# Kernel tuning notes

Hardware: AMD Instinct MI355X
Metric: run time of the kernel (lower is better)

## Reference

```python
import jax, jax.numpy as jnp
import numpy as np

N_C = 50000
N_N = 50000
E = 500000
D = 128


def _graph_conv(x_src, src, dst, n_src, n_dst, W, b):
    # DGL GraphConv, norm='both': symmetric degree normalization, then linear.
    ones = jnp.ones(src.shape, x_src.dtype)
    deg_out = jax.ops.segment_sum(ones, src, num_segments=n_src)
    deg_in = jax.ops.segment_sum(ones, dst, num_segments=n_dst)
    norm_src = jnp.maximum(deg_out, 1.0) ** -0.5  # [n_src]
    norm_dst = jnp.maximum(deg_in, 1.0) ** -0.5   # [n_dst]
    m = (x_src * norm_src[:, None])[src]          # [E, D] gather
    agg = jax.ops.segment_sum(m, dst, num_segments=n_dst)  # [n_dst, D]
    return (agg * norm_dst[:, None]) @ W + b


def _sage_conv(x_src, x_dst, src, dst, n_dst, W_self, W_neigh, b):
    # DGL SAGEConv, aggregator='mean': fc_self(h_dst) + fc_neigh(mean_neigh) + bias.
    ones = jnp.ones(src.shape, x_src.dtype)
    deg_in = jnp.maximum(jax.ops.segment_sum(ones, dst, num_segments=n_dst), 1.0)
    h_neigh = jax.ops.segment_sum(x_src[src], dst, num_segments=n_dst) / deg_in[:, None]
    return x_dst @ W_self + h_neigh @ W_neigh + b


def setup_inputs() -> dict:
    key = jax.random.key(0)
    ks = jax.random.split(key, 20)
    s = 1.0 / np.sqrt(D)
    inp = {
        'feat_C': jax.random.normal(ks[0], (N_C, D), jnp.float32),
        'feat_N': jax.random.normal(ks[1], (N_N, D), jnp.float32),
        'W1_cc': jax.random.normal(ks[2], (D, D), jnp.float32) * s,
        'b1_cc': jnp.zeros((D,), jnp.float32),
        'W1_cn': jax.random.normal(ks[3], (D, D), jnp.float32) * s,
        'b1_cn': jnp.zeros((D,), jnp.float32),
        'W1_self': jax.random.normal(ks[4], (D, D), jnp.float32) * s,
        'W1_neigh': jax.random.normal(ks[5], (D, D), jnp.float32) * s,
        'b1_nn': jnp.zeros((D,), jnp.float32),
        'W2_cc': jax.random.normal(ks[6], (D, D), jnp.float32) * s,
        'b2_cc': jnp.zeros((D,), jnp.float32),
        'W2_cn': jax.random.normal(ks[7], (D, D), jnp.float32) * s,
        'b2_cn': jnp.zeros((D,), jnp.float32),
        'W2_self': jax.random.normal(ks[8], (D, D), jnp.float32) * s,
        'W2_neigh': jax.random.normal(ks[9], (D, D), jnp.float32) * s,
        'b2_nn': jnp.zeros((D,), jnp.float32),
        'cc_src': jax.random.randint(ks[10], (E,), 0, N_C),
        'cc_dst': jax.random.randint(ks[11], (E,), 0, N_C),
        'cn_src': jax.random.randint(ks[12], (E,), 0, N_C),
        'cn_dst': jax.random.randint(ks[13], (E,), 0, N_N),
        'nn_src': jax.random.randint(ks[14], (E,), 0, N_N),
        'nn_dst': jax.random.randint(ks[15], (E,), 0, N_N),
    }
    return inp


def reference(feat_C, feat_N, W1_cc, b1_cc, W1_cn, b1_cn, W1_self, W1_neigh, b1_nn,
              W2_cc, b2_cc, W2_cn, b2_cn, W2_self, W2_neigh, b2_nn,
              cc_src, cc_dst, cn_src, cn_dst, nn_src, nn_dst):
    # layer 1 (HeteroGraphConv, aggregate='sum') + relu
    hC = _graph_conv(feat_C, cc_src, cc_dst, N_C, N_C, W1_cc, b1_cc)
    hN = (_graph_conv(feat_C, cn_src, cn_dst, N_C, N_N, W1_cn, b1_cn)
          + _sage_conv(feat_N, feat_N, nn_src, nn_dst, N_N, W1_self, W1_neigh, b1_nn))
    hC = jax.nn.relu(hC)
    hN = jax.nn.relu(hN)
    # layer 2
    oC = _graph_conv(hC, cc_src, cc_dst, N_C, N_C, W2_cc, b2_cc)
    oN = (_graph_conv(hC, cn_src, cn_dst, N_C, N_N, W2_cn, b2_cn)
          + _sage_conv(hN, hN, nn_src, nn_dst, N_N, W2_self, W2_neigh, b2_nn))
    return oC, oN
```

## Files before the change

kernel.cpp:

```cpp
#include <hip/hip_runtime.h>

#define NCN 50000
#define NE  500000
#define DF  128

#define BSHIFT 9
#define NBUCK 98
#define BK 128
#define CAP 7168
#define CHUNK 4096

typedef __attribute__((ext_vector_type(8))) short mfrag;
typedef __attribute__((ext_vector_type(4))) float facc4;

__device__ inline ushort f2bf(float x) {
    unsigned u = __float_as_uint(x);
    unsigned r = (u + 0x7FFFu + ((u >> 16) & 1u)) >> 16;
    return (ushort)r;
}
__device__ inline float bf2f(ushort h) { return __uint_as_float(((unsigned)h) << 16); }

__device__ inline void store_split(ushort* __restrict__ T, int row, int lane,
                                   float vx, float vy) {
    ushort hx = f2bf(vx); ushort lx = f2bf(vx - bf2f(hx));
    ushort hy = f2bf(vy); ushort ly = f2bf(vy - bf2f(hy));
    uint hp = (uint)hx | ((uint)hy << 16);
    uint lp = (uint)lx | ((uint)ly << 16);
    *(uint*)(T + (size_t)row * DF + lane * 2) = hp;
    *(uint*)(T + (size_t)NCN * DF + (size_t)row * DF + lane * 2) = lp;
}

__global__ __launch_bounds__(256) void binA_k(
    const int* __restrict__ cc_src, const int* __restrict__ cc_dst,
    const int* __restrict__ cn_src, const int* __restrict__ cn_dst,
    const int* __restrict__ nn_src, const int* __restrict__ nn_dst,
    uint2* __restrict__ R, int* __restrict__ bc)
{
    const int s = blockIdx.y;
    const int* key; const int* pay;
    switch (s) {
      case 0: key = cc_dst; pay = cc_src; break;
      case 1: key = cn_dst; pay = cn_src; break;
      case 2: key = nn_dst; pay = nn_src; break;
      case 3: key = cc_src; pay = nullptr; break;
      default: key = cn_src; pay = nullptr; break;
    }
    __shared__ uint2 rec[CHUNK];
    __shared__ int lhist[BK], lofs[BK], lcur[BK], gbase[BK];
    __shared__ int ls[256];
    const int tid = threadIdx.x;
    const int base = blockIdx.x * CHUNK;

    int k[16], p[16];
    #pragma unroll
    for (int j = 0; j < 16; ++j) {
        int e = base + j * 256 + tid;
        bool valid = (e < NE);
        k[j] = valid ? key[e] : -1;
        p[j] = (valid && pay) ? pay[e] : 0;
    }
    if (tid < BK) lhist[tid] = 0;
    __syncthreads();
    #pragma unroll
    for (int j = 0; j < 16; ++j)
        if (k[j] >= 0) atomicAdd(&lhist[k[j] >> BSHIFT], 1);
    __syncthreads();
    int v = (tid < BK) ? lhist[tid] : 0;
    ls[tid] = v;
    __syncthreads();
    #pragma unroll
    for (int off = 1; off < 128; off <<= 1) {
        int t = (tid >= off) ? ls[tid - off] : 0;
        __syncthreads();
        ls[tid] += t;
        __syncthreads();
    }
    if (tid < BK) { int e = ls[tid] - v; lofs[tid] = e; lcur[tid] = e; }
    __syncthreads();
    #pragma unroll
    for (int j = 0; j < 16; ++j) {
        if (k[j] >= 0) {
            int b = k[j] >> BSHIFT;
            int pos = atomicAdd(&lcur[b], 1);
            rec[pos] = make_uint2((unsigned)k[j], (unsigned)p[j]);
        }
    }
    __syncthreads();
    if (tid < BK) {
        int c = lcur[tid] - lofs[tid];
        gbase[tid] = (c > 0) ? atomicAdd(&bc[s * BK + tid], c) : 0;
    }
    __syncthreads();
    int total = ls[127];
    for (int i = tid; i < total; i += 256) {
        uint2 r = rec[i];
        int b = (int)(r.x >> BSHIFT);
        int gi = gbase[b] + (i - lofs[b]);
        R[((size_t)s * NBUCK + b) * CAP + gi] = r;
    }
}

__global__ __launch_bounds__(256) void binB_k(
    const uint2* __restrict__ R, const int* __restrict__ bc,
    int* __restrict__ rp3, int* __restrict__ col3, float* __restrict__ snorm2)
{
    const int b = blockIdx.x;
    const int s = blockIdx.y;
    const int tid = threadIdx.x;
    __shared__ int cnt[512];
    __shared__ int lofs[512];
    __shared__ int ls[256];
    __shared__ int sbase;

    const int nrec = bc[s * BK + b];
    const uint2* rec = R + ((size_t)s * NBUCK + b) * CAP;

    for (int i = tid; i < 512; i += 256) cnt[i] = 0;
    __syncthreads();
    for (int i = tid; i < nrec; i += 256)
        atomicAdd(&cnt[rec[i].x & 511], 1);
    __syncthreads();

    if (s >= 3) {
        float* sn = snorm2 + (size_t)(s - 3) * NCN;
        for (int j = tid; j < 512; j += 256) {
            int d = b * 512 + j;
            if (d < NCN) { int c = cnt[j]; if (c < 1) c = 1; sn[d] = rsqrtf((float)c); }
        }
        return;
    }

    {
        int v = (tid < b) ? bc[s * BK + tid] : 0;
        ls[tid] = v;
        __syncthreads();
        for (int off = 128; off > 0; off >>= 1) {
            if (tid < off) ls[tid] += ls[tid + off];
            __syncthreads();
        }
        if (tid == 0) sbase = ls[0];
        __syncthreads();
    }
    const int colBase = sbase;

    int v0 = cnt[2 * tid], v1 = cnt[2 * tid + 1];
    int pairSum = v0 + v1;
    ls[tid] = pairSum;
    __syncthreads();
    #pragma unroll
    for (int off = 1; off < 256; off <<= 1) {
        int t = (tid >= off) ? ls[tid - off] : 0;
        __syncthreads();
        ls[tid] += t;
        __syncthreads();
    }
    int excl = ls[tid] - pairSum;
    lofs[2 * tid] = excl;
    lofs[2 * tid + 1] = excl + v0;
    __syncthreads();
    const int total = ls[255];

    int* rp = rp3 + (size_t)s * (NCN + 1);
    for (int j = tid; j < 512; j += 256) {
        int d = b * 512 + j;
        if (d < NCN) rp[d] = colBase + lofs[j];
    }
    if (b == NBUCK - 1 && tid == 0) rp[NCN] = colBase + total;
    __syncthreads();

    int* col = col3 + (size_t)s * NE + colBase;
    for (int i = tid; i < nrec; i += 256) {
        uint2 r = rec[i];
        int pos = atomicAdd(&lofs[r.x & 511], 1);
        col[pos] = (int)r.y;
    }
}

__global__ __launch_bounds__(256) void wconv_k(
    const float* __restrict__ Wm0, const float* __restrict__ Wm1,
    const float* __restrict__ Wm2, const float* __restrict__ Wm3,
    const float* __restrict__ Wm4, const float* __restrict__ Wm5,
    const float* __restrict__ Wm6, const float* __restrict__ Wm7,
    ushort* __restrict__ out)
{
    const float* Ws[8] = {Wm0, Wm1, Wm2, Wm3, Wm4, Wm5, Wm6, Wm7};
    const float* W = Ws[blockIdx.x];
    ushort* o = out + (size_t)blockIdx.x * 32768;
    for (int i = threadIdx.x; i < 16384; i += 256) {
        int c = i >> 13;
        int r = i & 8191;
        int n = r >> 6;
        int jj = r & 63;
        int kk = c * 64 + (jj ^ ((n & 7) << 3));
        float wv = W[kk * 128 + n];
        ushort h = f2bf(wv);
        float lv = wv - bf2f(h);
        o[c * 16384 + r] = h;
        o[c * 16384 + 8192 + r] = f2bf(lv);
    }
}

__global__ __launch_bounds__(256) void agg2_k(
    const float* __restrict__ X,
    const int* __restrict__ rpA, const int* __restrict__ colA,
    const float* __restrict__ scA, ushort* __restrict__ outA,
    const int* __restrict__ rpB, const int* __restrict__ colB,
    const float* __restrict__ scB, ushort* __restrict__ outB)
{
    const int* rp; const int* col; const float* sc; ushort* out;
    if (blockIdx.y == 0) { rp = rpA; col = colA; sc = scA; out = outA; }
    else                 { rp = rpB; col = colB; sc = scB; out = outB; }
    int gid = blockIdx.x * 256 + threadIdx.x;
    int row = gid >> 6;
    int lane = threadIdx.x & 63;
    if (row >= NCN) return;
    int e0 = rp[row], e1 = rp[row + 1];
    float ax = 0.f, ay = 0.f;
    int e = e0;
    for (; e + 4 <= e1; e += 4) {
        int s0 = col[e], s1 = col[e + 1], s2 = col[e + 2], s3 = col[e + 3];
        float c0 = sc[s0], c1 = sc[s1], c2 = sc[s2], c3 = sc[s3];
        const float2 u0 = *(const float2*)(X + (size_t)s0 * DF + lane * 2);
        const float2 u1 = *(const float2*)(X + (size_t)s1 * DF + lane * 2);
        const float2 u2 = *(const float2*)(X + (size_t)s2 * DF + lane * 2);
        const float2 u3 = *(const float2*)(X + (size_t)s3 * DF + lane * 2);
        ax = fmaf(u0.x, c0, ax); ay = fmaf(u0.y, c0, ay);
        ax = fmaf(u1.x, c1, ax); ay = fmaf(u1.y, c1, ay);
        ax = fmaf(u2.x, c2, ax); ay = fmaf(u2.y, c2, ay);
        ax = fmaf(u3.x, c3, ax); ay = fmaf(u3.y, c3, ay);
    }
    for (; e < e1; ++e) {
        int s0 = col[e];
        float c0 = sc[s0];
        const float2 u0 = *(const float2*)(X + (size_t)s0 * DF + lane * 2);
        ax = fmaf(u0.x, c0, ax); ay = fmaf(u0.y, c0, ay);
    }
    int deg = e1 - e0; if (deg < 1) deg = 1;
    float dsc = rsqrtf((float)deg);
    store_split(out, row, lane, ax * dsc, ay * dsc);
}

__global__ __launch_bounds__(256) void agg1_k(
    const float* __restrict__ X, const int* __restrict__ rp,
    const int* __restrict__ col, ushort* __restrict__ out)
{
    int gid = blockIdx.x * 256 + threadIdx.x;
    int row = gid >> 6;
    int lane = threadIdx.x & 63;
    if (row >= NCN) return;
    int e0 = rp[row], e1 = rp[row + 1];
    float ax = 0.f, ay = 0.f;
    int e = e0;
    for (; e + 4 <= e1; e += 4) {
        int s0 = col[e], s1 = col[e + 1], s2 = col[e + 2], s3 = col[e + 3];
        const float2 u0 = *(const float2*)(X + (size_t)s0 * DF + lane * 2);
        const float2 u1 = *(const float2*)(X + (size_t)s1 * DF + lane * 2);
        const float2 u2 = *(const float2*)(X + (size_t)s2 * DF + lane * 2);
        const float2 u3 = *(const float2*)(X + (size_t)s3 * DF + lane * 2);
        ax += u0.x + u1.x + u2.x + u3.x;
        ay += u0.y + u1.y + u2.y + u3.y;
    }
    for (; e < e1; ++e) {
        int s0 = col[e];
        const float2 u0 = *(const float2*)(X + (size_t)s0 * DF + lane * 2);
        ax += u0.x; ay += u0.y;
    }
    int deg = e1 - e0; if (deg < 1) deg = 1;
    float dsc = 1.0f / (float)deg;
    store_split(out, row, lane, ax * dsc, ay * dsc);
}

template<int NSRC, bool RELU, int F32S>
__global__ __launch_bounds__(256, 3) void mgemm_k(
    const void* __restrict__ A0, const void* __restrict__ A1, const void* __restrict__ A2,
    const ushort* __restrict__ Wi0, const ushort* __restrict__ Wi1, const ushort* __restrict__ Wi2,
    const float* __restrict__ b0, const float* __restrict__ b1,
    float* __restrict__ Y, int M)
{
    constexpr int NCH = 2 * NSRC;
    __shared__ ushort Wsm[16384];
    const int tid = threadIdx.x;
    const int l = tid & 63;
    const int wv = tid >> 6;
    const int r0 = blockIdx.x * 128;

    const void*   Aarr[3] = {A0, A1, A2};
    const ushort* Warr[3] = {Wi0, Wi1, Wi2};

    int arow[2];
    #pragma unroll
    for (int rt = 0; rt < 2; ++rt) {
        int r = r0 + wv * 32 + rt * 16 + (l & 15);
        arow[rt] = (r < M) ? r : (M - 1);
    }
    const int kgrp = (l >> 4) * 8;

    facc4 acc[2][8];
    #pragma unroll
    for (int rt = 0; rt < 2; ++rt)
        #pragma unroll
        for (int ct = 0; ct < 8; ++ct)
            acc[rt][ct] = (facc4){0.f, 0.f, 0.f, 0.f};

    uint4 Wr[8];
    auto loadWr = [&](int c) {
        int s = c >> 1, half = c & 1;
        const uint4* wp = (const uint4*)(Warr[s] + half * 16384);
        #pragma unroll
        for (int i = 0; i < 8; ++i) Wr[i] = wp[i * 256 + tid];
    };

    mfrag ah[2][2], al[2][2];
    auto loadA = [&](int c) {
        int s = c >> 1;
        int k0 = (c & 1) * 64;
        if (s == F32S) {
            const float* F = (const float*)Aarr[s];
            #pragma unroll
            for (int ks = 0; ks < 2; ++ks)
                #pragma unroll
                for (int rt = 0; rt < 2; ++rt) {
                    const float* p = F + (size_t)arow[rt] * DF + k0 + ks * 32 + kgrp;
                    float4 v0 = *(const float4*)p;
                    float4 v1 = *(const float4*)(p + 4);
                    union { mfrag m; ushort u[8]; } H, L;
                    float vv0[4] = {v0.x, v0.y, v0.z, v0.w};
                    float vv1[4] = {v1.x, v1.y, v1.z, v1.w};
                    #pragma unroll
                    for (int j = 0; j < 4; ++j) {
                        ushort h = f2bf(vv0[j]);
                        H.u[j] = h; L.u[j] = f2bf(vv0[j] - bf2f(h));
                    }
                    #pragma unroll
                    for (int j = 0; j < 4; ++j) {
                        ushort h = f2bf(vv1[j]);
                        H.u[4 + j] = h; L.u[4 + j] = f2bf(vv1[j] - bf2f(h));
                    }
                    ah[ks][rt] = H.m; al[ks][rt] = L.m;
                }
        } else {
            const ushort* T = (const ushort*)Aarr[s];
            #pragma unroll
            for (int ks = 0; ks < 2; ++ks)
                #pragma unroll
                for (int rt = 0; rt < 2; ++rt) {
                    size_t o = (size_t)arow[rt] * DF + k0 + ks * 32 + kgrp;
                    ah[ks][rt] = *(const mfrag*)(T + o);
                    al[ks][rt] = *(const mfrag*)(T + (size_t)NCN * DF + o);
                }
        }
    };

    loadWr(0);
    #pragma unroll
    for (int c = 0; c < NCH; ++c) {
        __syncthreads();
        {
            uint4* wd = (uint4*)Wsm;
            #pragma unroll
            for (int i = 0; i < 8; ++i) wd[i * 256 + tid] = Wr[i];
        }
        loadA(c);
        if (c + 1 < NCH) loadWr(c + 1);
        __syncthreads();
        #pragma unroll
        for (int ks = 0; ks < 2; ++ks) {
            const int kbyte = ks * 64 + (l >> 4) * 16;
            #pragma unroll
            for (int ct = 0; ct < 8; ++ct) {
                int colc = ct * 16 + (l & 15);
                int widx = colc * 64 + ((kbyte ^ ((colc & 7) << 4)) >> 1);
                mfrag w_hi = *(const mfrag*)(Wsm + widx);
                mfrag w_lo = *(const mfrag*)(Wsm + 8192 + widx);
                #pragma unroll
                for (int rt = 0; rt < 2; ++rt) {
                    acc[rt][ct] = __builtin_amdgcn_mfma_f32_16x16x32_bf16(ah[ks][rt], w_hi, acc[rt][ct], 0, 0, 0);
                    acc[rt][ct] = __builtin_amdgcn_mfma_f32_16x16x32_bf16(ah[ks][rt], w_lo, acc[rt][ct], 0, 0, 0);
                    acc[rt][ct] = __builtin_amdgcn_mfma_f32_16x16x32_bf16(al[ks][rt], w_hi, acc[rt][ct], 0, 0, 0);
                }
            }
        }
    }

    float bias[8];
    #pragma unroll
    for (int ct = 0; ct < 8; ++ct) {
        int colc = ct * 16 + (l & 15);
        float bv = b0 ? b0[colc] : 0.f;
        if (b1) bv += b1[colc];
        bias[ct] = bv;
    }
    #pragma unroll
    for (int rt = 0; rt < 2; ++rt) {
        #pragma unroll
        for (int q = 0; q < 4; ++q) {
            int row = r0 + wv * 32 + rt * 16 + (l >> 4) * 4 + q;
            if (row < M) {
                #pragma unroll
                for (int ct = 0; ct < 8; ++ct) {
                    float v = acc[rt][ct][q] + bias[ct];
                    if (RELU) v = fmaxf(v, 0.f);
                    Y[(size_t)row * DF + ct * 16 + (l & 15)] = v;
                }
            }
        }
    }
}

extern "C" void kernel_launch(void* const* d_in, const int* in_sizes, int n_in,
                              void* d_out, int out_size, void* d_ws, size_t ws_size,
                              hipStream_t stream)
{
    (void)in_sizes; (void)n_in; (void)out_size; (void)ws_size;
    const float* feat_C   = (const float*)d_in[0];
    const float* feat_N   = (const float*)d_in[1];
    const float* W1_cc    = (const float*)d_in[2];
    const float* b1_cc    = (const float*)d_in[3];
    const float* W1_cn    = (const float*)d_in[4];
    const float* b1_cn    = (const float*)d_in[5];
    const float* W1_self  = (const float*)d_in[6];
    const float* W1_neigh = (const float*)d_in[7];
    const float* b1_nn    = (const float*)d_in[8];
    const float* W2_cc    = (const float*)d_in[9];
    const float* b2_cc    = (const float*)d_in[10];
    const float* W2_cn    = (const float*)d_in[11];
    const float* b2_cn    = (const float*)d_in[12];
    const float* W2_self  = (const float*)d_in[13];
    const float* W2_neigh = (const float*)d_in[14];
    const float* b2_nn    = (const float*)d_in[15];
    const int* cc_src = (const int*)d_in[16];
    const int* cc_dst = (const int*)d_in[17];
    const int* cn_src = (const int*)d_in[18];
    const int* cn_dst = (const int*)d_in[19];
    const int* nn_src = (const int*)d_in[20];
    const int* nn_dst = (const int*)d_in[21];

    char* ws = (char*)d_ws;
    size_t off = 0;
    auto take = [&](size_t bytes) -> char* {
        char* p = ws + off;
        off = (off + bytes + 255) & ~(size_t)255;
        return p;
    };
    int*    rp3    = (int*)take((size_t)3 * (NCN + 1) * sizeof(int));
    int*    col3   = (int*)take((size_t)3 * NE * sizeof(int));
    float*  snorm2 = (float*)take((size_t)2 * NCN * sizeof(float));
    int*    bc     = (int*)take((size_t)5 * BK * sizeof(int));
    ushort* Wimg   = (ushort*)take((size_t)8 * 32768 * sizeof(ushort));
    char* bigRegion = take((size_t)2 * 2 * NCN * DF * sizeof(ushort));
    uint2*  R  = (uint2*)bigRegion;
    ushort* P0 = (ushort*)bigRegion;
    ushort* P1 = (ushort*)(bigRegion + (size_t)2 * NCN * DF * sizeof(ushort));

    float* oC = (float*)d_out;
    float* oN = oC + (size_t)NCN * DF;

    const int binABlocks = (NE + CHUNK - 1) / CHUNK;
    const int aggBlocks  = (NCN * 64 + 255) / 256;
    const int gemmBlocks = (NCN + 127) / 128;

    auto img = [&](int m) { return (const ushort*)(Wimg + (size_t)m * 32768); };
    const int* rpCC = rp3 + 0 * (NCN + 1);
    const int* rpCN = rp3 + 1 * (NCN + 1);
    const int* rpNN = rp3 + 2 * (NCN + 1);
    const int* colCC = col3 + 0 * NE;
    const int* colCN = col3 + 1 * NE;
    const int* colNN = col3 + 2 * NE;
    const float* snCC = snorm2 + 0 * NCN;
    const float* snCN = snorm2 + 1 * NCN;

    hipMemsetAsync(bc, 0, (size_t)5 * BK * sizeof(int), stream);
    binA_k<<<dim3(binABlocks, 5), 256, 0, stream>>>(cc_src, cc_dst, cn_src, cn_dst,
                                                    nn_src, nn_dst, R, bc);
    binB_k<<<dim3(NBUCK, 5), 256, 0, stream>>>(R, bc, rp3, col3, snorm2);
    wconv_k<<<8, 256, 0, stream>>>(W1_cc, W1_cn, W1_neigh, W1_self,
                                   W2_cc, W2_cn, W2_neigh, W2_self, Wimg);

    agg2_k<<<dim3(aggBlocks, 2), 256, 0, stream>>>(feat_C,
                                                   rpCC, colCC, snCC, P0,
                                                   rpCN, colCN, snCN, P1);
    mgemm_k<1, true, -1><<<gemmBlocks, 256, 0, stream>>>(P0, nullptr, nullptr,
                                                         img(0), nullptr, nullptr,
                                                         b1_cc, nullptr, oC, NCN);
    agg1_k<<<aggBlocks, 256, 0, stream>>>(feat_N, rpNN, colNN, P0);
    mgemm_k<3, true, 2><<<gemmBlocks, 256, 0, stream>>>(P1, P0, feat_N,
                                                        img(1), img(2), img(3),
                                                        b1_cn, b1_nn, oN, NCN);

    agg2_k<<<dim3(aggBlocks, 2), 256, 0, stream>>>(oC,
                                                   rpCN, colCN, snCN, P1,
                                                   rpCC, colCC, snCC, P0);
    mgemm_k<1, false, -1><<<gemmBlocks, 256, 0, stream>>>(P0, nullptr, nullptr,
                                                          img(4), nullptr, nullptr,
                                                          b2_cc, nullptr, oC, NCN);
    agg1_k<<<aggBlocks, 256, 0, stream>>>(oN, rpNN, colNN, P0);
    mgemm_k<3, false, 2><<<gemmBlocks, 256, 0, stream>>>(P1, P0, oN,
                                                         img(5), img(6), img(7),
                                                         b2_cn, b2_nn, oN, NCN);
}
```

Before: 416.4 us.

## Merge aggregation launches, stage NN aggregate in output buffer, separate source-degree histogram

Source-degree normalization now comes from a dedicated atomic histogram kernel instead of two extra binning passes, so the bin kernels handle only the three destination-keyed edge sets. The three layer-1 aggregations are fused into one 3-way launch. The NN mean aggregate is staged as a split-bf16 buffer inside the still-unused oC output region, so everything runs before the GEMMs and the CN+SAGE GEMM goes before the CC GEMM. mgemm occupancy is raised to 4 blocks and a barrier is added before the epilogue. The ordering is fragile: layer 2 reads oC as input and later writes it, and the oCsplit buffer must not overlap the data it reads.

```diff
diff --git a/kernel.cpp b/kernel.cpp
--- a/kernel.cpp
+++ b/kernel.cpp
@@ -30,6 +30,25 @@
     *(uint*)(T + (size_t)NCN * DF + (size_t)row * DF + lane * 2) = lp;
 }
 
+__global__ __launch_bounds__(256) void hist2_k(
+    const int* __restrict__ cc_src, const int* __restrict__ cn_src,
+    int* __restrict__ cnt2)
+{
+    int i = blockIdx.x * 256 + threadIdx.x;
+    if (i >= NE) return;
+    atomicAdd(&cnt2[cc_src[i]], 1);
+    atomicAdd(&cnt2[NCN + cn_src[i]], 1);
+}
+
+__global__ __launch_bounds__(256) void srcnorm_k(
+    const int* __restrict__ cnt2, float* __restrict__ snorm2, int n2)
+{
+    int i = blockIdx.x * 256 + threadIdx.x;
+    if (i >= n2) return;
+    int c = cnt2[i]; if (c < 1) c = 1;
+    snorm2[i] = rsqrtf((float)c);
+}
+
 __global__ __launch_bounds__(256) void binA_k(
     const int* __restrict__ cc_src, const int* __restrict__ cc_dst,
     const int* __restrict__ cn_src, const int* __restrict__ cn_dst,
@@ -41,9 +60,7 @@
     switch (s) {
       case 0: key = cc_dst; pay = cc_src; break;
       case 1: key = cn_dst; pay = cn_src; break;
-      case 2: key = nn_dst; pay = nn_src; break;
-      case 3: key = cc_src; pay = nullptr; break;
-      default: key = cn_src; pay = nullptr; break;
+      default: key = nn_dst; pay = nn_src; break;
     }
     __shared__ uint2 rec[CHUNK];
     __shared__ int lhist[BK], lofs[BK], lcur[BK], gbase[BK];
@@ -57,7 +74,7 @@
         int e = base + j * 256 + tid;
         bool valid = (e < NE);
         k[j] = valid ? key[e] : -1;
-        p[j] = (valid && pay) ? pay[e] : 0;
+        p[j] = valid ? pay[e] : 0;
     }
     if (tid < BK) lhist[tid] = 0;
     __syncthreads();
@@ -102,7 +119,7 @@
 
 __global__ __launch_bounds__(256) void binB_k(
     const uint2* __restrict__ R, const int* __restrict__ bc,
-    int* __restrict__ rp3, int* __restrict__ col3, float* __restrict__ snorm2)
+    int* __restrict__ rp3, int* __restrict__ col3)
 {
     const int b = blockIdx.x;
     const int s = blockIdx.y;
@@ -120,15 +137,6 @@
     for (int i = tid; i < nrec; i += 256)
         atomicAdd(&cnt[rec[i].x & 511], 1);
     __syncthreads();
-
-    if (s >= 3) {
-        float* sn = snorm2 + (size_t)(s - 3) * NCN;
-        for (int j = tid; j < 512; j += 256) {
-            int d = b * 512 + j;
-            if (d < NCN) { int c = cnt[j]; if (c < 1) c = 1; sn[d] = rsqrtf((float)c); }
-        }
-        return;
-    }
 
     {
         int v = (tid < b) ? bc[s * BK + tid] : 0;
@@ -200,16 +208,22 @@
     }
 }
 
-__global__ __launch_bounds__(256) void agg2_k(
-    const float* __restrict__ X,
-    const int* __restrict__ rpA, const int* __restrict__ colA,
-    const float* __restrict__ scA, ushort* __restrict__ outA,
-    const int* __restrict__ rpB, const int* __restrict__ colB,
-    const float* __restrict__ scB, ushort* __restrict__ outB)
-{
-    const int* rp; const int* col; const float* sc; ushort* out;
-    if (blockIdx.y == 0) { rp = rpA; col = colA; sc = scA; out = outA; }
-    else                 { rp = rpB; col = colB; sc = scB; out = outB; }
+__global__ __launch_bounds__(256) void agg_k(
+    const float* __restrict__ X0, const int* __restrict__ rp0,
+    const int* __restrict__ col0, const float* __restrict__ sc0,
+    ushort* __restrict__ out0,
+    const float* __restrict__ X1, const int* __restrict__ rp1,
+    const int* __restrict__ col1, const float* __restrict__ sc1,
+    ushort* __restrict__ out1,
+    const float* __restrict__ X2, const int* __restrict__ rp2,
+    const int* __restrict__ col2, const float* __restrict__ sc2,
+    ushort* __restrict__ out2)
+{
+    const float* X; const int* rp; const int* col; const float* sc; ushort* out;
+    if (blockIdx.y == 0)      { X = X0; rp = rp0; col = col0; sc = sc0; out = out0; }
+    else if (blockIdx.y == 1) { X = X1; rp = rp1; col = col1; sc = sc1; out = out1; }
+    else                      { X = X2; rp = rp2; col = col2; sc = sc2; out = out2; }
+
     int gid = blockIdx.x * 256 + threadIdx.x;
     int row = gid >> 6;
     int lane = threadIdx.x & 63;
@@ -219,7 +233,10 @@
     int e = e0;
     for (; e + 4 <= e1; e += 4) {
         int s0 = col[e], s1 = col[e + 1], s2 = col[e + 2], s3 = col[e + 3];
-        float c0 = sc[s0], c1 = sc[s1], c2 = sc[s2], c3 = sc[s3];
+        float c0 = sc ? sc[s0] : 1.0f;
+        float c1 = sc ? sc[s1] : 1.0f;
+        float c2 = sc ? sc[s2] : 1.0f;
+        float c3 = sc ? sc[s3] : 1.0f;
         const float2 u0 = *(const float2*)(X + (size_t)s0 * DF + lane * 2);
         const float2 u1 = *(const float2*)(X + (size_t)s1 * DF + lane * 2);
         const float2 u2 = *(const float2*)(X + (size_t)s2 * DF + lane * 2);
@@ -231,47 +248,17 @@
     }
     for (; e < e1; ++e) {
         int s0 = col[e];
-        float c0 = sc[s0];
+        float c0 = sc ? sc[s0] : 1.0f;
         const float2 u0 = *(const float2*)(X + (size_t)s0 * DF + lane * 2);
         ax = fmaf(u0.x, c0, ax); ay = fmaf(u0.y, c0, ay);
     }
     int deg = e1 - e0; if (deg < 1) deg = 1;
-    float dsc = rsqrtf((float)deg);
+    float dsc = sc ? rsqrtf((float)deg) : (1.0f / (float)deg);
     store_split(out, row, lane, ax * dsc, ay * dsc);
 }
 
-__global__ __launch_bounds__(256) void agg1_k(
-    const float* __restrict__ X, const int* __restrict__ rp,
-    const int* __restrict__ col, ushort* __restrict__ out)
-{
-    int gid = blockIdx.x * 256 + threadIdx.x;
-    int row = gid >> 6;
-    int lane = threadIdx.x & 63;
-    if (row >= NCN) return;
-    int e0 = rp[row], e1 = rp[row + 1];
-    float ax = 0.f, ay = 0.f;
-    int e = e0;
-    for (; e + 4 <= e1; e += 4) {
-        int s0 = col[e], s1 = col[e + 1], s2 = col[e + 2], s3 = col[e + 3];
-        const float2 u0 = *(const float2*)(X + (size_t)s0 * DF + lane * 2);
-        const float2 u1 = *(const float2*)(X + (size_t)s1 * DF + lane * 2);
-        const float2 u2 = *(const float2*)(X + (size_t)s2 * DF + lane * 2);
-        const float2 u3 = *(const float2*)(X + (size_t)s3 * DF + lane * 2);
-        ax += u0.x + u1.x + u2.x + u3.x;
-        ay += u0.y + u1.y + u2.y + u3.y;
-    }
-    for (; e < e1; ++e) {
-        int s0 = col[e];
-        const float2 u0 = *(const float2*)(X + (size_t)s0 * DF + lane * 2);
-        ax += u0.x; ay += u0.y;
-    }
-    int deg = e1 - e0; if (deg < 1) deg = 1;
-    float dsc = 1.0f / (float)deg;
-    store_split(out, row, lane, ax * dsc, ay * dsc);
-}
-
 template<int NSRC, bool RELU, int F32S>
-__global__ __launch_bounds__(256, 3) void mgemm_k(
+__global__ __launch_bounds__(256, 4) void mgemm_k(
     const void* __restrict__ A0, const void* __restrict__ A1, const void* __restrict__ A2,
     const ushort* __restrict__ Wi0, const ushort* __restrict__ Wi1, const ushort* __restrict__ Wi2,
     const float* __restrict__ b0, const float* __restrict__ b1,
@@ -381,6 +368,7 @@
             }
         }
     }
+    __syncthreads();
 
     float bias[8];
     #pragma unroll
@@ -445,7 +433,8 @@
     int*    rp3    = (int*)take((size_t)3 * (NCN + 1) * sizeof(int));
     int*    col3   = (int*)take((size_t)3 * NE * sizeof(int));
     float*  snorm2 = (float*)take((size_t)2 * NCN * sizeof(float));
-    int*    bc     = (int*)take((size_t)5 * BK * sizeof(int));
+    int*    cnt2   = (int*)take((size_t)2 * NCN * sizeof(int));
+    int*    bc     = (int*)take((size_t)3 * BK * sizeof(int));
     ushort* Wimg   = (ushort*)take((size_t)8 * 32768 * sizeof(ushort));
     char* bigRegion = take((size_t)2 * 2 * NCN * DF * sizeof(ushort));
     uint2*  R  = (uint2*)bigRegion;
@@ -454,7 +443,9 @@
 
     float* oC = (float*)d_out;
     float* oN = oC + (size_t)NCN * DF;
-
+    ushort* oCsplit = (ushort*)oC;
+
+    const int edgeBlocks = (NE + 255) / 256;
     const int binABlocks = (NE + CHUNK - 1) / CHUNK;
     const int aggBlocks  = (NCN * 64 + 255) / 256;
     const int gemmBlocks = (NCN + 127) / 128;
@@ -469,32 +460,39 @@
     const float* snCC = snorm2 + 0 * NCN;
     const float* snCN = snorm2 + 1 * NCN;
 
-    hipMemsetAsync(bc, 0, (size_t)5 * BK * sizeof(int), stream);
-    binA_k<<<dim3(binABlocks, 5), 256, 0, stream>>>(cc_src, cc_dst, cn_src, cn_dst,
+    hipMemsetAsync(cnt2, 0, (size_t)2 * NCN * sizeof(int), stream);
+    hipMemsetAsync(bc, 0, (size_t)3 * BK * sizeof(int), stream);
+    hist2_k<<<edgeBlocks, 256, 0, stream>>>(cc_src, cn_src, cnt2);
+    srcnorm_k<<<(2 * NCN + 255) / 256, 256, 0, stream>>>(cnt2, snorm2, 2 * NCN);
+    binA_k<<<dim3(binABlocks, 3), 256, 0, stream>>>(cc_src, cc_dst, cn_src, cn_dst,
                                                     nn_src, nn_dst, R, bc);
-    binB_k<<<dim3(NBUCK, 5), 256, 0, stream>>>(R, bc, rp3, col3, snorm2);
+    binB_k<<<dim3(NBUCK, 3), 256, 0, stream>>>(R, bc, rp3, col3);
     wconv_k<<<8, 256, 0, stream>>>(W1_cc, W1_cn, W1_neigh, W1_self,
                                    W2_cc, W2_cn, W2_neigh, W2_self, Wimg);
 
-    agg2_k<<<dim3(aggBlocks, 2), 256, 0, stream>>>(feat_C,
-                                                   rpCC, colCC, snCC, P0,
-                                                   rpCN, colCN, snCN, P1);
+    agg_k<<<dim3(aggBlocks, 3), 256, 0, stream>>>(
+        feat_C, rpCC, colCC, snCC, P0,
+        feat_C, rpCN, colCN, snCN, P1,
+        feat_N, rpNN, colNN, nullptr, oCsplit);
+    mgemm_k<3, true, 2><<<gemmBlocks, 256, 0, stream>>>(P1, oCsplit, feat_N,
+                                                        img(1), img(2), img(3),
+                                                        b1_cn, b1_nn, oN, NCN);
     mgemm_k<1, true, -1><<<gemmBlocks, 256, 0, stream>>>(P0, nullptr, nullptr,
                                                          img(0), nullptr, nullptr,
                                                          b1_cc, nullptr, oC, NCN);
-    agg1_k<<<aggBlocks, 256, 0, stream>>>(feat_N, rpNN, colNN, P0);
-    mgemm_k<3, true, 2><<<gemmBlocks, 256, 0, stream>>>(P1, P0, feat_N,
-                                                        img(1), img(2), img(3),
-                                                        b1_cn, b1_nn, oN, NCN);
-
-    agg2_k<<<dim3(aggBlocks, 2), 256, 0, stream>>>(oC,
-                                                   rpCN, colCN, snCN, P1,
-                                                   rpCC, colCC, snCC, P0);
+
+    agg_k<<<dim3(aggBlocks, 2), 256, 0, stream>>>(
+        oC, rpCC, colCC, snCC, P0,
+        oC, rpCN, colCN, snCN, P1,
+        nullptr, nullptr, nullptr, nullptr, nullptr);
+    agg_k<<<dim3(aggBlocks, 1), 256, 0, stream>>>(
+        oN, rpNN, colNN, nullptr, oCsplit,
+        nullptr, nullptr, nullptr, nullptr, nullptr,
+        nullptr, nullptr, nullptr, nullptr, nullptr);
+    mgemm_k<3, false, 2><<<gemmBlocks, 256, 0, stream>>>(P1, oCsplit, oN,
+                                                         img(5), img(6), img(7),
+                                                         b2_cn, b2_nn, oN, NCN);
     mgemm_k<1, false, -1><<<gemmBlocks, 256, 0, stream>>>(P0, nullptr, nullptr,
                                                           img(4), nullptr, nullptr,
                                                           b2_cc, nullptr, oC, NCN);
-    agg1_k<<<aggBlocks, 256, 0, stream>>>(oN, rpNN, colNN, P0);
-    mgemm_k<3, false, 2><<<gemmBlocks, 256, 0, stream>>>(P1, P0, oN,
-                                                         img(5), img(6), img(7),
-                                                         b2_cn, b2_nn, oN, NCN);
-}
+}
```

Result: slower. 485.2 us (+16.5%).
